# Optimization experiments

Measured on AMD Instinct MI355X. Metric: run time of the kernel, lower is better.

The kernel has to match this reference:

```python
import jax, jax.numpy as jnp
import numpy as np

DIM_IN, DIM_K, DIM_V = 1024, 1024, 1024

def setup_inputs() -> dict:
    key = jax.random.key(0)
    k1, k2, k3, k4 = jax.random.split(key, 4)
    x = jax.random.normal(k1, (4, 2048, DIM_IN), dtype=jnp.float32)
    # Linear(dim_in, dim_k, bias=False): store as [in, out] for x @ W
    Wq = jax.random.normal(k2, (DIM_IN, DIM_K), dtype=jnp.float32) * (1.0 / np.sqrt(DIM_IN))
    Wk = jax.random.normal(k3, (DIM_IN, DIM_K), dtype=jnp.float32) * (1.0 / np.sqrt(DIM_IN))
    Wv = jax.random.normal(k4, (DIM_IN, DIM_V), dtype=jnp.float32) * (1.0 / np.sqrt(DIM_IN))
    return {"x": x, "Wq": Wq, "Wk": Wk, "Wv": Wv, "causal_mask": 1}

def reference(x, Wq, Wk, Wv, causal_mask):
    # x: [b, n, dim_in]
    b, n, _ = x.shape
    q = jnp.einsum('bnd,dk->bnk', x, Wq)
    k = jnp.einsum('bnd,dk->bnk', x, Wk)
    v = jnp.einsum('bnd,dv->bnv', x, Wv)
    scale = 1.0 / np.sqrt(Wq.shape[1])
    dist = jnp.einsum('bik,bjk->bij', q, k) * scale  # [b, n, n]
    if causal_mask:
        mask = jnp.tril(jnp.ones((n, n), dtype=bool))
        dist = jnp.where(mask, dist, -jnp.inf)
    attn = jax.nn.softmax(dist, axis=-1)
    return jnp.einsum('bij,bjv->biv', attn, v)  # [b, n, dim_v]
```

## Files before the change

kernel.cpp:

```cpp
#include <hip/hip_runtime.h>
#include <hip/hip_bf16.h>
#include <stdint.h>

#define BM 128
#define BN 128
#define BK 64

typedef __attribute__((ext_vector_type(8))) short bf16x8;
typedef __attribute__((ext_vector_type(4))) float floatx4;


__device__ __forceinline__ unsigned short f2bf(float f) {
    unsigned int x;
    __builtin_memcpy(&x, &f, 4);
    unsigned int r = (x + 0x7fffu + ((x >> 16) & 1u)) >> 16;
    return (unsigned short)r;
}

__device__ __forceinline__ float bf2f_hi(unsigned int u_hi_masked) {
    float f;
    __builtin_memcpy(&f, &u_hi_masked, 4);
    return f;
}

__device__ __forceinline__ void async_copy16(const void* g, void* l) {
    __builtin_amdgcn_global_load_lds(
        (const __attribute__((address_space(1))) void*)(uintptr_t)g,
        (__attribute__((address_space(3))) void*)(uint32_t)(uintptr_t)l,
        16, 0, 0);
}


__global__ __launch_bounds__(256) void prep(const float* __restrict__ x,
                                            const float* __restrict__ Wq,
                                            const float* __restrict__ Wk,
                                            const float* __restrict__ Wv,
                                            unsigned short* __restrict__ xb,
                                            unsigned short* __restrict__ wT) {
    __shared__ float tile[32][33];
    int bid = blockIdx.x;
    int tid = threadIdx.x;
    if (bid < 8192) {
        int i = bid * 256 + tid;
        float4 v = ((const float4*)x)[i];
        ushort4 o;
        o.x = f2bf(v.x);
        o.y = f2bf(v.y);
        o.z = f2bf(v.z);
        o.w = f2bf(v.w);
        ((ushort4*)xb)[i] = o;
    } else {
        int w = bid - 8192;
        int z = w >> 10;
        int r = w & 1023;
        int bx = (r & 31) * 32;
        int by = (r >> 5) * 32;
        const float* W = z == 0 ? Wq : (z == 1 ? Wk : Wv);
        int tx = tid & 31, ty = tid >> 5;
        for (int rr = 0; rr < 32; rr += 8)
            tile[ty + rr][tx] = W[(size_t)(by + ty + rr) * 1024 + bx + tx];
        __syncthreads();
        unsigned short* o = wT + (size_t)z * 1024 * 1024;
        for (int rr = 0; rr < 32; rr += 8)
            o[(size_t)(bx + ty + rr) * 1024 + by + tx] = f2bf(tile[tx][ty + rr]);
    }
}


#define SEG_STRIDE 544
#define BUF_SH (16 * SEG_STRIDE)


__device__ __forceinline__ void gemm_core(const unsigned short* __restrict__ A,
                                          int lda,
                                          const unsigned short* __restrict__ B,
                                          int ldb, void* __restrict__ C,
                                          int ldc, bool out_bf16, int kend,
                                          float scale, int m0, int n0) {
    __shared__ __align__(16) unsigned short As[BUF_SH];
    __shared__ __align__(16) unsigned short Bs[BUF_SH];

    int tid = threadIdx.x;
    int lane = tid & 63;
    int wave = tid >> 6;
    int wm = (wave >> 1) * 64;
    int wn = (wave & 1) * 64;
    int fr = lane & 15;
    int kq = lane >> 4;

    floatx4 acc[4][4] = {};

    for (int k0 = 0; k0 < kend; k0 += BK) {
#pragma unroll
        for (int q = 0; q < 4; q++) {
            int s = 4 * q + wave;
            int r = s * 8 + (lane >> 3);
            int ko = (lane & 7) * 8;
            int dst = s * SEG_STRIDE + lane * 8;
            async_copy16(A + (size_t)(m0 + r) * lda + k0 + ko, &As[dst]);
            async_copy16(B + (size_t)(n0 + r) * ldb + k0 + ko, &Bs[dst]);
        }
        __syncthreads();

#pragma unroll
        for (int kh = 0; kh < 2; kh++) {
            int kc = kh * 4 + kq;
            bf16x8 af[4], bfg[4];
#pragma unroll
            for (int mi = 0; mi < 4; mi++) {
                int row = wm + mi * 16 + fr;
                af[mi] = *(const bf16x8*)&As[(row >> 3) * SEG_STRIDE +
                                             (row & 7) * 64 + kc * 8];
            }
#pragma unroll
            for (int ni = 0; ni < 4; ni++) {
                int row = wn + ni * 16 + fr;
                bfg[ni] = *(const bf16x8*)&Bs[(row >> 3) * SEG_STRIDE +
                                              (row & 7) * 64 + kc * 8];
            }
#pragma unroll
            for (int mi = 0; mi < 4; mi++)
#pragma unroll
                for (int ni = 0; ni < 4; ni++)
                    acc[mi][ni] = __builtin_amdgcn_mfma_f32_16x16x32_bf16(
                        af[mi], bfg[ni], acc[mi][ni], 0, 0, 0);
        }
        __syncthreads();
    }

    int col0 = n0 + wn + fr;
    int rbase = m0 + wm + kq * 4;
    if (out_bf16) {
        unsigned short* Cb = (unsigned short*)C;
#pragma unroll
        for (int mi = 0; mi < 4; mi++)
#pragma unroll
            for (int ni = 0; ni < 4; ni++)
#pragma unroll
                for (int r = 0; r < 4; r++)
                    Cb[(size_t)(rbase + mi * 16 + r) * ldc + col0 + ni * 16] =
                        f2bf(acc[mi][ni][r] * scale);
    } else {
        float* Cb = (float*)C;
#pragma unroll
        for (int mi = 0; mi < 4; mi++)
#pragma unroll
            for (int ni = 0; ni < 4; ni++)
#pragma unroll
                for (int r = 0; r < 4; r++)
                    Cb[(size_t)(rbase + mi * 16 + r) * ldc + col0 + ni * 16] =
                        acc[mi][ni][r] * scale;
    }
}


__device__ __forceinline__ void gemm_core_db(
    const unsigned short* __restrict__ A, int lda,
    const unsigned short* __restrict__ B, int ldb, void* __restrict__ C,
    int ldc, bool out_bf16, int kend, float scale, int m0, int n0) {
    __shared__ __align__(16) unsigned short As[2 * BUF_SH];
    __shared__ __align__(16) unsigned short Bs[2 * BUF_SH];

    int tid = threadIdx.x;
    int lane = tid & 63;
    int wave = tid >> 6;
    int wm = (wave >> 1) * 64;
    int wn = (wave & 1) * 64;
    int fr = lane & 15;
    int kq = lane >> 4;

    floatx4 acc[4][4] = {};

    auto stage = [&](int buf, int k0) {
#pragma unroll
        for (int q = 0; q < 4; q++) {
            int s = 4 * q + wave;
            int r = s * 8 + (lane >> 3);
            int ko = (lane & 7) * 8;
            int dst = buf * BUF_SH + s * SEG_STRIDE + lane * 8;
            async_copy16(A + (size_t)(m0 + r) * lda + k0 + ko, &As[dst]);
            async_copy16(B + (size_t)(n0 + r) * ldb + k0 + ko, &Bs[dst]);
        }
    };

    auto compute = [&](int buf) {
        const unsigned short* as = &As[buf * BUF_SH];
        const unsigned short* bs = &Bs[buf * BUF_SH];
#pragma unroll
        for (int kh = 0; kh < 2; kh++) {
            int kc = kh * 4 + kq;
            bf16x8 af[4], bfg[4];
#pragma unroll
            for (int mi = 0; mi < 4; mi++) {
                int row = wm + mi * 16 + fr;
                af[mi] = *(const bf16x8*)&as[(row >> 3) * SEG_STRIDE +
                                             (row & 7) * 64 + kc * 8];
            }
#pragma unroll
            for (int ni = 0; ni < 4; ni++) {
                int row = wn + ni * 16 + fr;
                bfg[ni] = *(const bf16x8*)&bs[(row >> 3) * SEG_STRIDE +
                                              (row & 7) * 64 + kc * 8];
            }
#pragma unroll
            for (int mi = 0; mi < 4; mi++)
#pragma unroll
                for (int ni = 0; ni < 4; ni++)
                    acc[mi][ni] = __builtin_amdgcn_mfma_f32_16x16x32_bf16(
                        af[mi], bfg[ni], acc[mi][ni], 0, 0, 0);
        }
    };

    stage(0, 0);
    __syncthreads();
    int nt = kend / BK;
    int cur = 0;
    for (int t = 0; t < nt; t++) {
        if (t + 1 < nt) stage(cur ^ 1, (t + 1) * BK);
        compute(cur);
        __syncthreads();
        cur ^= 1;
    }

    int col0 = n0 + wn + fr;
    int rbase = m0 + wm + kq * 4;
    if (out_bf16) {
        unsigned short* Cb = (unsigned short*)C;
#pragma unroll
        for (int mi = 0; mi < 4; mi++)
#pragma unroll
            for (int ni = 0; ni < 4; ni++)
#pragma unroll
                for (int r = 0; r < 4; r++)
                    Cb[(size_t)(rbase + mi * 16 + r) * ldc + col0 + ni * 16] =
                        f2bf(acc[mi][ni][r] * scale);
    } else {
        float* Cb = (float*)C;
#pragma unroll
        for (int mi = 0; mi < 4; mi++)
#pragma unroll
            for (int ni = 0; ni < 4; ni++)
#pragma unroll
                for (int r = 0; r < 4; r++)
                    Cb[(size_t)(rbase + mi * 16 + r) * ldc + col0 + ni * 16] =
                        acc[mi][ni][r] * scale;
    }
}


__device__ __forceinline__ void tri_decode(int r2, int& mb, int& nb) {
    mb = (int)((sqrtf(8.0f * r2 + 1.0f) - 1.0f) * 0.5f);
    while ((mb + 1) * (mb + 2) / 2 <= r2) mb++;
    while (mb * (mb + 1) / 2 > r2) mb--;
    nb = r2 - mb * (mb + 1) / 2;
}


__global__ __launch_bounds__(256, 4) void gemm_qk(
    const unsigned short* __restrict__ xb, const unsigned short* __restrict__ wT,
    unsigned short* __restrict__ qk) {
    gemm_core(xb, 1024, wT, 1024, qk, 2048, true, 1024, 1.0f,
              blockIdx.y * BM, blockIdx.x * BN);
}


__global__ __launch_bounds__(256, 4) void gemm_s(
    const unsigned short* __restrict__ qk, unsigned short* __restrict__ S) {
    int bz = blockIdx.x / 136;
    int mb, nb;
    tri_decode(blockIdx.x - bz * 136, mb, nb);
    const unsigned short* Q = qk + (size_t)bz * 2048 * 2048;
    gemm_core(Q, 2048, Q + 1024, 2048, S + (size_t)bz * 2048 * 2048, 2048,
              true, 1024, 0.03125f, mb * BM, nb * BN);
}


__global__ __launch_bounds__(256, 4) void sm_vt(
    unsigned short* __restrict__ S, const unsigned short* __restrict__ wTv,
    const unsigned short* __restrict__ xb, unsigned short* __restrict__ vt) {
    int bid = blockIdx.x;
    if (bid < 512) {
        gemm_core_db(wTv, 1024, xb, 1024, vt, 8192, true, 1024, 1.0f,
                     (bid >> 6) * BM, (bid & 63) * BN);
        return;
    }
    int lane = threadIdx.x & 63;
    int row = (bid - 512) * 4 + (threadIdx.x >> 6);
    int i = row & 2047;
    unsigned short* s = S + (size_t)row * 2048;

    uint4 raw[4];
#pragma unroll
    for (int c = 0; c < 4; c++) raw[c] = ((const uint4*)s)[lane + c * 64];

    const float NEG = -1.0e30f;
    float p[32];
    float m = NEG;
#pragma unroll
    for (int c = 0; c < 4; c++) {
        const unsigned int* u = (const unsigned int*)&raw[c];
#pragma unroll
        for (int w = 0; w < 4; w++) {
            int j = c * 512 + lane * 8 + w * 2;
            float f0 = bf2f_hi(u[w] << 16);
            float f1 = bf2f_hi(u[w] & 0xffff0000u);
            f0 = (j <= i) ? f0 : NEG;
            f1 = (j + 1 <= i) ? f1 : NEG;
            p[c * 8 + w * 2] = f0;
            p[c * 8 + w * 2 + 1] = f1;
            m = fmaxf(m, fmaxf(f0, f1));
        }
    }
#pragma unroll
    for (int o = 32; o > 0; o >>= 1) m = fmaxf(m, __shfl_xor(m, o));

    float sum = 0.f;
#pragma unroll
    for (int t = 0; t < 32; t++) {
        p[t] = __expf(p[t] - m);
        sum += p[t];
    }
#pragma unroll
    for (int o = 32; o > 0; o >>= 1) sum += __shfl_xor(sum, o);
    float inv = 1.0f / sum;

#pragma unroll
    for (int c = 0; c < 4; c++) {
        uint4 out;
        unsigned int* u = (unsigned int*)&out;
#pragma unroll
        for (int w = 0; w < 4; w++) {
            unsigned int lo = f2bf(p[c * 8 + w * 2] * inv);
            unsigned int hi = f2bf(p[c * 8 + w * 2 + 1] * inv);
            u[w] = lo | (hi << 16);
        }
        ((uint4*)s)[lane + c * 64] = out;
    }
}


__global__ __launch_bounds__(256, 4) void gemm_pv(
    const unsigned short* __restrict__ S, const unsigned short* __restrict__ vt,
    float* __restrict__ out) {
    int b = blockIdx.x;
    int j = b < 256 ? b : 767 - b;
    int mb = j >> 5;
    int rem = j & 31;
    int bz = rem >> 3, nb = rem & 7;
    int kend = (mb + 1) * 128;
    gemm_core_db(S + (size_t)bz * 2048 * 2048, 2048, vt + (size_t)bz * 2048,
                 8192, out + (size_t)bz * 2048 * 1024, 1024, false, kend, 1.0f,
                 mb * BM, nb * BN);
}


extern "C" void kernel_launch(void* const* d_in, const int* in_sizes, int n_in,
                              void* d_out, int out_size, void* d_ws,
                              size_t ws_size, hipStream_t stream) {
    const float* x = (const float*)d_in[0];
    const float* Wq = (const float*)d_in[1];
    const float* Wk = (const float*)d_in[2];
    const float* Wv = (const float*)d_in[3];

    char* ws = (char*)d_ws;
    unsigned short* qk = (unsigned short*)(ws);
    unsigned short* S = (unsigned short*)(ws + 33554432);
    unsigned short* vt = (unsigned short*)(ws + 67108864);
    unsigned short* xb = (unsigned short*)(ws + 83886080);
    unsigned short* wT = (unsigned short*)(ws + 100663296);

    prep<<<11264, 256, 0, stream>>>(x, Wq, Wk, Wv, xb, wT);
    gemm_qk<<<dim3(16, 64), 256, 0, stream>>>(xb, wT, qk);
    gemm_s<<<544, 256, 0, stream>>>(qk, S);
    sm_vt<<<2560, 256, 0, stream>>>(S, wT + 2 * 1024 * 1024, xb, vt);
    gemm_pv<<<512, 256, 0, stream>>>(S, vt, (float*)d_out);
}
```

Before: 238.3 us.

## Replace QK projection GEMM with 256x256-tile 8-wave pipelined kernel

The Q/K projection GEMM now uses a dedicated kernel with 256x256 output tiles, 512 threads (8 waves), and a 4-deep LDS ring of async copies. Loads for A and B are interleaved with two MFMA half-phases, and explicit vmcnt waits and barriers replace the generic core. Wave priority is raised around the MFMA bursts. The aim is more data reuse per tile and better overlap of global loads with compute. The cost is a smaller grid (256 blocks), higher register pressure and more fragile hand scheduling.

```diff
diff --git a/kernel.cpp b/kernel.cpp
--- a/kernel.cpp
+++ b/kernel.cpp
@@ -248,19 +248,126 @@
 }
 
 
+__global__ __launch_bounds__(512, 2) void gemm_qk8(
+    const unsigned short* __restrict__ A, const unsigned short* __restrict__ B,
+    unsigned short* __restrict__ C) {
+    __shared__ __align__(16) unsigned short lds[4][16384];
+
+    const int tid = threadIdx.x;
+    const int lane = tid & 63;
+    const int wave = tid >> 6;
+    const int wr = wave >> 2;
+    const int wc = wave & 3;
+    const int fr = lane & 15;
+    const int kq = lane >> 4;
+    const int m0 = blockIdx.y * 256;
+    const int n0 = blockIdx.x * 256;
+
+    const unsigned short* aS0 =
+        A + (size_t)(m0 + wave * 32 + (lane >> 2)) * 1024 + (lane & 3) * 8;
+    const unsigned short* aS1 = aS0 + 16 * 1024;
+    const unsigned short* bS0 =
+        B + (size_t)(n0 + wave * 32 + (lane >> 2)) * 1024 + (lane & 3) * 8;
+    const unsigned short* bS1 = bS0 + 16 * 1024;
+    const int dA0 = wave * 2 * 512 + lane * 8;
+    const int dA1 = dA0 + 512;
+    const int dB0 = 8192 + dA0;
+    const int dB1 = 8192 + dA1;
+
+    floatx4 acc[8][4] = {};
+
+    auto stageA = [&](int j) {
+        unsigned short* d = &lds[j & 3][0];
+        int kk = j * 32;
+        async_copy16(aS0 + kk, d + dA0);
+        async_copy16(aS1 + kk, d + dA1);
+    };
+    auto stageB = [&](int j) {
+        unsigned short* d = &lds[j & 3][0];
+        int kk = j * 32;
+        async_copy16(bS0 + kk, d + dB0);
+        async_copy16(bS1 + kk, d + dB1);
+    };
+
+    stageA(0); stageB(0);
+    stageA(1); stageB(1);
+    stageA(2); stageB(2);
+    asm volatile("s_waitcnt vmcnt(8)" ::: "memory");
+    __builtin_amdgcn_s_barrier();
+    __builtin_amdgcn_sched_barrier(0);
+
+    for (int j = 0; j < 32; ++j) {
+        const unsigned short* as = &lds[j & 3][0];
+        const unsigned short* bs = as + 8192;
+        bf16x8 af[4], bfr[4];
+
+#pragma unroll
+        for (int mi = 0; mi < 4; mi++)
+            af[mi] = *(const bf16x8*)&as[(wr * 128 + mi * 16 + fr) * 32 + kq * 8];
+#pragma unroll
+        for (int ni = 0; ni < 4; ni++)
+            bfr[ni] = *(const bf16x8*)&bs[(wc * 64 + ni * 16 + fr) * 32 + kq * 8];
+        if (j + 3 < 32) stageA(j + 3);
+        __builtin_amdgcn_s_barrier();
+        __builtin_amdgcn_sched_barrier(0);
+        __builtin_amdgcn_s_setprio(1);
+#pragma unroll
+        for (int mi = 0; mi < 4; mi++)
+#pragma unroll
+            for (int ni = 0; ni < 4; ni++)
+                acc[mi][ni] = __builtin_amdgcn_mfma_f32_16x16x32_bf16(
+                    af[mi], bfr[ni], acc[mi][ni], 0, 0, 0);
+        __builtin_amdgcn_s_setprio(0);
+        __builtin_amdgcn_s_barrier();
+        __builtin_amdgcn_sched_barrier(0);
+
+#pragma unroll
+        for (int mi = 0; mi < 4; mi++)
+            af[mi] = *(const bf16x8*)&as[(wr * 128 + 64 + mi * 16 + fr) * 32 +
+                                         kq * 8];
+#pragma unroll
+        for (int ni = 0; ni < 4; ni++)
+            bfr[ni] = *(const bf16x8*)&bs[(wc * 64 + ni * 16 + fr) * 32 + kq * 8];
+        if (j + 3 < 32) stageB(j + 3);
+        if (j <= 28) {
+            asm volatile("s_waitcnt vmcnt(8)" ::: "memory");
+        } else if (j == 29) {
+            asm volatile("s_waitcnt vmcnt(4)" ::: "memory");
+        } else if (j == 30) {
+            asm volatile("s_waitcnt vmcnt(0)" ::: "memory");
+        }
+        __builtin_amdgcn_s_barrier();
+        __builtin_amdgcn_sched_barrier(0);
+        __builtin_amdgcn_s_setprio(1);
+#pragma unroll
+        for (int mi = 0; mi < 4; mi++)
+#pragma unroll
+            for (int ni = 0; ni < 4; ni++)
+                acc[4 + mi][ni] = __builtin_amdgcn_mfma_f32_16x16x32_bf16(
+                    af[mi], bfr[ni], acc[4 + mi][ni], 0, 0, 0);
+        __builtin_amdgcn_s_setprio(0);
+        __builtin_amdgcn_s_barrier();
+        __builtin_amdgcn_sched_barrier(0);
+    }
+
+    const int col0 = n0 + wc * 64 + fr;
+    const int rbase = m0 + wr * 128 + kq * 4;
+#pragma unroll
+    for (int a = 0; a < 8; a++)
+#pragma unroll
+        for (int ni = 0; ni < 4; ni++)
+#pragma unroll
+            for (int r = 0; r < 4; r++)
+                C[(size_t)(rbase + a * 16 + r) * 2048 + col0 + ni * 16] =
+                    f2bf(acc[a][ni][r]);
+}
+
+
 __device__ __forceinline__ void tri_decode(int r2, int& mb, int& nb) {
     mb = (int)((sqrtf(8.0f * r2 + 1.0f) - 1.0f) * 0.5f);
     while ((mb + 1) * (mb + 2) / 2 <= r2) mb++;
     while (mb * (mb + 1) / 2 > r2) mb--;
     nb = r2 - mb * (mb + 1) / 2;
-}
-
-
-__global__ __launch_bounds__(256, 4) void gemm_qk(
-    const unsigned short* __restrict__ xb, const unsigned short* __restrict__ wT,
-    unsigned short* __restrict__ qk) {
-    gemm_core(xb, 1024, wT, 1024, qk, 2048, true, 1024, 1.0f,
-              blockIdx.y * BM, blockIdx.x * BN);
 }
 
 
@@ -370,7 +477,7 @@
     unsigned short* wT = (unsigned short*)(ws + 100663296);
 
     prep<<<11264, 256, 0, stream>>>(x, Wq, Wk, Wv, xb, wT);
-    gemm_qk<<<dim3(16, 64), 256, 0, stream>>>(xb, wT, qk);
+    gemm_qk8<<<dim3(8, 32), 512, 0, stream>>>(xb, wT, qk);
     gemm_s<<<544, 256, 0, stream>>>(qk, S);
     sm_vt<<<2560, 256, 0, stream>>>(S, wT + 2 * 1024 * 1024, xb, vt);
     gemm_pv<<<512, 256, 0, stream>>>(S, vt, (float*)d_out);
```

Measured after the change: 243.6 us. 1.02x slower.
